# Optimization experiments

Measured on AMD Instinct MI355X. Metric: run time of the kernel, lower is better.

Reference implementation:

```python
import jax, jax.numpy as jnp
import numpy as np

N_NODES = 50000
N_EDGES = 800000
N_GRAPHS = 64
IN_C = 64
HID = 64
HEADS = 4
NEG_SLOPE = 0.2
EPS = 1e-16


def setup_inputs() -> dict:
    key = jax.random.key(0)
    ks = jax.random.split(key, 16)
    x = jax.random.normal(ks[0], (N_NODES, IN_C), dtype=jnp.float32)
    edge_index = jax.random.randint(ks[1], (2, N_EDGES), 0, N_NODES, dtype=jnp.int64)
    batch = jnp.sort(jax.random.randint(ks[2], (N_NODES,), 0, N_GRAPHS, dtype=jnp.int64))
    s = 1.0 / np.sqrt(IN_C)
    s2 = 1.0 / np.sqrt(HID * HEADS)
    s3 = 1.0 / np.sqrt(HID)
    return {
        "x": x,
        "edge_index": edge_index,
        "batch": batch,
        # GATv2 layer 1: in 64 -> heads*64 = 256 (concat)
        "Wl1": jax.random.normal(ks[3], (IN_C, HEADS * HID), dtype=jnp.float32) * s,
        "Wr1": jax.random.normal(ks[4], (IN_C, HEADS * HID), dtype=jnp.float32) * s,
        "att1": jax.random.normal(ks[5], (HEADS, HID), dtype=jnp.float32) * s3,
        "b1": jnp.zeros((HEADS * HID,), dtype=jnp.float32),
        # GATv2 layer 2: in 256 -> 1 head * 64
        "Wl2": jax.random.normal(ks[6], (HEADS * HID, HID), dtype=jnp.float32) * s2,
        "Wr2": jax.random.normal(ks[7], (HEADS * HID, HID), dtype=jnp.float32) * s2,
        "att2": jax.random.normal(ks[8], (1, HID), dtype=jnp.float32) * s3,
        "b2": jnp.zeros((HID,), dtype=jnp.float32),
        # MLP head: 64 -> 64 -> 2
        "W3": jax.random.normal(ks[9], (HID, 64), dtype=jnp.float32) * s3,
        "b3": jnp.zeros((64,), dtype=jnp.float32),
        "W4": jax.random.normal(ks[10], (64, 2), dtype=jnp.float32) * (1.0 / 8.0),
        "b4": jnp.zeros((2,), dtype=jnp.float32),
    }


def gatv2_conv(x, src, dst, Wl, Wr, att, bias, heads, out_c, n_nodes):
    # PyG GATv2Conv (eval mode, add_self_loops=False, concat heads):
    # x_l = lin_l(x) used for SOURCE nodes (messages), x_r = lin_r(x) for TARGET nodes.
    xl = (x @ Wl).reshape(n_nodes, heads, out_c)
    xr = (x @ Wr).reshape(n_nodes, heads, out_c)
    e = jax.nn.leaky_relu(xl[src] + xr[dst], NEG_SLOPE)          # [E, H, C]
    logits = jnp.einsum('ehc,hc->eh', e, att)                    # [E, H]
    # numerically stable softmax over incoming edges of each target node
    m = jax.ops.segment_max(logits, dst, num_segments=n_nodes)   # [N, H]
    ex = jnp.exp(logits - m[dst])
    denom = jax.ops.segment_sum(ex, dst, num_segments=n_nodes)   # [N, H]
    alpha = ex / (denom[dst] + EPS)                              # [E, H]
    out = jax.ops.segment_sum(alpha[:, :, None] * xl[src], dst, num_segments=n_nodes)
    return out.reshape(n_nodes, heads * out_c) + bias


def reference(x, edge_index, batch, Wl1, Wr1, att1, b1, Wl2, Wr2, att2, b2, W3, b3, W4, b4):
    src, dst = edge_index[0], edge_index[1]
    n = x.shape[0]
    h = gatv2_conv(x, src, dst, Wl1, Wr1, att1, b1, HEADS, HID, n)
    h = jax.nn.elu(h)
    h = gatv2_conv(h, src, dst, Wl2, Wr2, att2, b2, 1, HID, n)
    h = jax.nn.elu(h)
    # global mean pool over graphs
    sums = jax.ops.segment_sum(h, batch, num_segments=N_GRAPHS)
    cnt = jax.ops.segment_sum(jnp.ones((n,), dtype=h.dtype), batch, num_segments=N_GRAPHS)
    pooled = sums / jnp.maximum(cnt, 1.0)[:, None]
    # MLP head (dropout inactive in eval)
    z = jax.nn.relu(pooled @ W3 + b3)
    return z @ W4 + b4
```

## Files before the change

kernel.cpp:

```cpp
#include <hip/hip_runtime.h>
#include <hip/hip_fp16.h>
#include <math.h>

#define N_NODES 50000
#define N_EDGES 800000
#define N_GRAPHS 64
#define L2E 1.44269504f

#if __has_builtin(__builtin_amdgcn_fdot2)
#define HAS_FDOT2 1
typedef _Float16 h2_t __attribute__((ext_vector_type(2)));
#else
#define HAS_FDOT2 0
#endif

typedef _Float16 f16x8 __attribute__((ext_vector_type(8)));
typedef float f32x4 __attribute__((ext_vector_type(4)));

__device__ __forceinline__ float elu1(float v){ return v > 0.f ? v : expm1f(v); }

__device__ __forceinline__ float pkdot(float4 q, const __half2* r2,
        const __half2* A6, const __half2* A4){
    const __half2* qh = (const __half2*)&q;
    float p = 0.f;
#if HAS_FDOT2
    #pragma unroll
    for (int i=0;i<4;i++){
        __half2 u = __hadd2(qh[i], r2[i]);
        __half2 ua = __builtin_bit_cast(__half2,
            __builtin_bit_cast(unsigned, u) & 0x7FFF7FFFu);
        p = __builtin_amdgcn_fdot2(__builtin_bit_cast(h2_t,u),
                                   __builtin_bit_cast(h2_t,A6[i]), p, false);
        p = __builtin_amdgcn_fdot2(__builtin_bit_cast(h2_t,ua),
                                   __builtin_bit_cast(h2_t,A4[i]), p, false);
    }
#else
    #pragma unroll
    for (int i=0;i<4;i++){
        float2 qf = __half22float2(qh[i]);
        float2 rf = __half22float2(r2[i]);
        float2 s6 = __half22float2(A6[i]);
        float2 s4 = __half22float2(A4[i]);
        float u0 = qf.x + rf.x, u1 = qf.y + rf.y;
        p = fmaf(s6.x, u0, fmaf(s4.x, fabsf(u0), p));
        p = fmaf(s6.y, u1, fmaf(s4.y, fabsf(u1), p));
    }
#endif
    return p;
}

__global__ __launch_bounds__(256) void k_prep(const float* __restrict__ x,
        const float* __restrict__ Wl1, const float* __restrict__ Wr1,
        const float* __restrict__ Wl2, const float* __restrict__ Wr2,
        const int* __restrict__ ei,
        __half* __restrict__ xh, __half* __restrict__ Wt1, __half* __restrict__ Wt2,
        int* __restrict__ deg, float* __restrict__ pooled){
    int t = threadIdx.x, bk = blockIdx.x;
    if (bk < 3125){
        int idx = bk*256 + t;
        float4 v = ((const float4*)x)[idx];
        __half2* dst = (__half2*)xh + (size_t)idx*2;
        dst[0] = __floats2half2_rn(v.x, v.y);
        dst[1] = __floats2half2_rn(v.z, v.w);
    } else if (bk < 3381){
        int elem = (bk-3125)*256 + t;
        if (elem < 32768){
            int c = elem >> 6, k = elem & 63;
            float v = (c < 256) ? Wl1[k*256 + c] : Wr1[k*256 + (c-256)];
            Wt1[elem] = __float2half(v);
        } else {
            int e2 = elem - 32768;
            int c = e2 >> 8, k = e2 & 255;
            float v = (c < 64) ? Wl2[k*64 + c] : Wr2[k*64 + (c-64)];
            Wt2[e2] = __float2half(v);
        }
        if (elem < N_GRAPHS*64) pooled[elem] = 0.f;
    } else {
        int e4 = (bk-3381)*256 + t;
        if (e4 < N_EDGES/4){
            int4 d = ((const int4*)(ei + N_EDGES))[e4];
            atomicAdd(&deg[d.x],1); atomicAdd(&deg[d.y],1);
            atomicAdd(&deg[d.z],1); atomicAdd(&deg[d.w],1);
        }
    }
}

__global__ __launch_bounds__(1024) void k_scan_a(const int* __restrict__ deg,
        int* __restrict__ rowptr, int* __restrict__ partial){
    __shared__ int s[1024];
    int t = threadIdx.x; int i = blockIdx.x*1024 + t;
    int v = (i < N_NODES) ? deg[i] : 0;
    s[t] = v; __syncthreads();
    for (int off=1; off<1024; off<<=1){
        int add = (t>=off) ? s[t-off] : 0;
        __syncthreads();
        s[t] += add;
        __syncthreads();
    }
    if (i < N_NODES) rowptr[i] = s[t] - v;
    if (t == 1023) partial[blockIdx.x] = s[1023];
}

__global__ __launch_bounds__(1024) void k_scan_c(int* __restrict__ rowptr,
        int* __restrict__ cursor, const int* __restrict__ partial){
    __shared__ int base;
    if (threadIdx.x == 0){
        int run = 0;
        for (int bk=0; bk<(int)blockIdx.x; bk++) run += partial[bk];
        base = run;
    }
    __syncthreads();
    int i = blockIdx.x*1024 + threadIdx.x;
    if (i < N_NODES){
        int r = rowptr[i] + base;
        rowptr[i] = r; cursor[i] = r;
    } else if (i == N_NODES){
        rowptr[N_NODES] = N_EDGES;
    }
}

__global__ void k_scatter(const int* __restrict__ ei, int* __restrict__ cursor,
                          int* __restrict__ srcs){
    int e4 = blockIdx.x*256 + threadIdx.x;
    if (e4 < N_EDGES/4){
        int4 sv = ((const int4*)ei)[e4];
        int4 dv = ((const int4*)(ei + N_EDGES))[e4];
        int p0 = atomicAdd(&cursor[dv.x],1); srcs[p0] = sv.x;
        int p1 = atomicAdd(&cursor[dv.y],1); srcs[p1] = sv.y;
        int p2 = atomicAdd(&cursor[dv.z],1); srcs[p2] = sv.z;
        int p3 = atomicAdd(&cursor[dv.w],1); srcs[p3] = sv.w;
    }
}

__global__ __launch_bounds__(256) void k_mm1(const __half* __restrict__ xh,
        const __half* __restrict__ Wt1,
        __half* __restrict__ xl1h, __half* __restrict__ xr1h){
    __shared__ __half lds[4][16*136];
    int w = threadIdx.x >> 6, l = threadIdx.x & 63;
    int r0 = blockIdx.x*64 + w*16;
    int cg = blockIdx.y;
    int lr = l & 15, lk = l >> 4, lk4 = lk*4;
    int ar = r0 + lr; if (ar >= N_NODES) ar = N_NODES-1;
    const __half* arow = xh + (size_t)ar*64;
    f16x8 a0 = *(const f16x8*)(arow + lk*8);
    f16x8 a1 = *(const f16x8*)(arow + 32 + lk*8);
    f32x4 acc[8];
    #pragma unroll
    for (int ct=0; ct<8; ct++) acc[ct] = (f32x4){0.f,0.f,0.f,0.f};
    #pragma unroll
    for (int ct=0; ct<8; ct++){
        int col = cg*128 + ct*16 + lr;
        const __half* brow = Wt1 + (size_t)col*64;
        f16x8 b0 = *(const f16x8*)(brow + lk*8);
        f16x8 b1 = *(const f16x8*)(brow + 32 + lk*8);
        acc[ct] = __builtin_amdgcn_mfma_f32_16x16x32_f16(a0, b0, acc[ct], 0,0,0);
        acc[ct] = __builtin_amdgcn_mfma_f32_16x16x32_f16(a1, b1, acc[ct], 0,0,0);
    }
    #pragma unroll
    for (int ct=0; ct<8; ct++){
        #pragma unroll
        for (int i=0;i<4;i++)
            lds[w][(lk4+i)*136 + ct*16 + lr] = __float2half(acc[ct][i]);
    }
    __half* base = (cg < 2) ? xl1h : xr1h;
    int cbase = (cg & 1)*128;
    #pragma unroll
    for (int rr=0; rr<4; rr++){
        int row = rr*4 + lk;
        float4 v = *(const float4*)&lds[w][row*136 + lr*8];
        int grow = r0 + row;
        if (grow < N_NODES)
            *(float4*)&base[(size_t)grow*256 + cbase + lr*8] = v;
    }
}

__global__ __launch_bounds__(256) void k_mm2(const __half* __restrict__ h1h,
        const __half* __restrict__ Wt2,
        __half* __restrict__ xl2h, __half* __restrict__ xr2h){
    __shared__ __half lds[4][16*72];
    int w = threadIdx.x >> 6, l = threadIdx.x & 63;
    int r0 = blockIdx.x*64 + w*16;
    int cg = blockIdx.y;
    int lr = l & 15, lk = l >> 4, lk4 = lk*4;
    int ar = r0 + lr; if (ar >= N_NODES) ar = N_NODES-1;
    const __half* arow = h1h + (size_t)ar*256;
    f32x4 acc[4];
    #pragma unroll
    for (int ct=0; ct<4; ct++) acc[ct] = (f32x4){0.f,0.f,0.f,0.f};
    #pragma unroll
    for (int ks=0; ks<8; ks++){
        f16x8 a = *(const f16x8*)(arow + ks*32 + lk*8);
        #pragma unroll
        for (int ct=0; ct<4; ct++){
            int col = cg*64 + ct*16 + lr;
            f16x8 bf = *(const f16x8*)(Wt2 + (size_t)col*256 + ks*32 + lk*8);
            acc[ct] = __builtin_amdgcn_mfma_f32_16x16x32_f16(a, bf, acc[ct], 0,0,0);
        }
    }
    #pragma unroll
    for (int ct=0; ct<4; ct++){
        #pragma unroll
        for (int i=0;i<4;i++)
            lds[w][(lk4+i)*72 + ct*16 + lr] = __float2half(acc[ct][i]);
    }
    __half* base = (cg == 0) ? xl2h : xr2h;
    #pragma unroll
    for (int rr=0; rr<2; rr++){
        int row = rr*8 + (l>>3);
        float4 v = *(const float4*)&lds[w][row*72 + (l&7)*8];
        int grow = r0 + row;
        if (grow < N_NODES)
            *(float4*)&base[(size_t)grow*64 + (l&7)*8] = v;
    }
}

__global__ __launch_bounds__(256) void k_gat1(const __half* __restrict__ xlh,
        const __half* __restrict__ xrh, const int* __restrict__ srcs,
        const int* __restrict__ rowptr, const float* __restrict__ att,
        const float* __restrict__ b, __half* __restrict__ h1h){
    int w = threadIdx.x >> 6, l = threadIdx.x & 63;
    int n = blockIdx.x*4 + w;
    int g = l >> 5, sub = l & 31;
    const float4* xh4 = (const float4*)xlh;
    float4 rq = *(const float4*)(xrh + (size_t)n*256 + sub*8);
    __half2 r2[4];
    { const __half2* rh = (const __half2*)&rq;
      r2[0]=rh[0]; r2[1]=rh[1]; r2[2]=rh[2]; r2[3]=rh[3]; }
    float4 A0v = *(const float4*)(att + sub*8);
    float4 A1v = *(const float4*)(att + sub*8 + 4);
    const float C6 = 0.6f*L2E, C4 = 0.4f*L2E;
    __half2 A6[4] = { __floats2half2_rn(A0v.x*C6, A0v.y*C6),
                      __floats2half2_rn(A0v.z*C6, A0v.w*C6),
                      __floats2half2_rn(A1v.x*C6, A1v.y*C6),
                      __floats2half2_rn(A1v.z*C6, A1v.w*C6) };
    __half2 A4[4] = { __floats2half2_rn(A0v.x*C4, A0v.y*C4),
                      __floats2half2_rn(A0v.z*C4, A0v.w*C4),
                      __floats2half2_rn(A1v.x*C4, A1v.y*C4),
                      __floats2half2_rn(A1v.z*C4, A1v.w*C4) };
    const __half2 Z2 = __floats2half2_rn(0.f, 0.f);
    float accf[8];
    #pragma unroll
    for (int c=0;c<8;c++) accf[c]=0.f;
    float dacc = 0.f;
    int beg = rowptr[n], end = rowptr[n+1];
    for (int j = beg; j < end; j += 8){
        int j0=j+g, j1=j+2+g, j2=j+4+g, j3=j+6+g;
        bool c0=j0<end, c1=j1<end, c2=j2<end, c3=j3<end;
        int s0 = c0 ? srcs[j0] : 0;
        int s1 = c1 ? srcs[j1] : 0;
        int s2 = c2 ? srcs[j2] : 0;
        int s3 = c3 ? srcs[j3] : 0;
        float4 q0 = xh4[(size_t)(unsigned)s0*32 + sub];
        float4 q1 = xh4[(size_t)(unsigned)s1*32 + sub];
        float4 q2 = xh4[(size_t)(unsigned)s2*32 + sub];
        float4 q3 = xh4[(size_t)(unsigned)s3*32 + sub];
        float p0 = pkdot(q0, r2, A6, A4);
        float p1 = pkdot(q1, r2, A6, A4);
        float p2 = pkdot(q2, r2, A6, A4);
        float p3 = pkdot(q3, r2, A6, A4);
        #pragma unroll
        for (int off=1; off<8; off<<=1){
            p0 += __shfl_xor(p0, off);
            p1 += __shfl_xor(p1, off);
            p2 += __shfl_xor(p2, off);
            p3 += __shfl_xor(p3, off);
        }
        float e0 = c0 ? exp2f(p0) : 0.f;
        float e1 = c1 ? exp2f(p1) : 0.f;
        float e2 = c2 ? exp2f(p2) : 0.f;
        float e3 = c3 ? exp2f(p3) : 0.f;
        __half2 E0 = __half2half2(__float2half_rn(e0));
        __half2 E1 = __half2half2(__float2half_rn(e1));
        __half2 E2 = __half2half2(__float2half_rn(e2));
        __half2 E3 = __half2half2(__float2half_rn(e3));
        const __half2* q0h = (const __half2*)&q0;
        const __half2* q1h = (const __half2*)&q1;
        const __half2* q2h = (const __half2*)&q2;
        const __half2* q3h = (const __half2*)&q3;
        #pragma unroll
        for (int i=0;i<4;i++){
            __half2 a16 = __hfma2(E0, q0h[i], Z2);
            a16 = __hfma2(E1, q1h[i], a16);
            a16 = __hfma2(E2, q2h[i], a16);
            a16 = __hfma2(E3, q3h[i], a16);
            float2 f = __half22float2(a16);
            accf[2*i]   += f.x;
            accf[2*i+1] += f.y;
        }
        dacc += e0 + e1 + e2 + e3;
    }
    #pragma unroll
    for (int c=0;c<8;c++) accf[c] += __shfl_xor(accf[c], 32);
    dacc += __shfl_xor(dacc, 32);
    if (l < 32){
        float inv = 1.f / (dacc + 1e-16f);
        float4 B0 = *(const float4*)(b + l*8);
        float4 B1 = *(const float4*)(b + l*8 + 4);
        float4 st;
        __half2* sp = (__half2*)&st;
        sp[0] = __floats2half2_rn(elu1(fmaf(accf[0],inv,B0.x)), elu1(fmaf(accf[1],inv,B0.y)));
        sp[1] = __floats2half2_rn(elu1(fmaf(accf[2],inv,B0.z)), elu1(fmaf(accf[3],inv,B0.w)));
        sp[2] = __floats2half2_rn(elu1(fmaf(accf[4],inv,B1.x)), elu1(fmaf(accf[5],inv,B1.y)));
        sp[3] = __floats2half2_rn(elu1(fmaf(accf[6],inv,B1.z)), elu1(fmaf(accf[7],inv,B1.w)));
        *(float4*)(h1h + (size_t)n*256 + l*8) = st;
    }
}

__global__ __launch_bounds__(256) void k_gat2(const __half* __restrict__ xlh,
        const __half* __restrict__ xrh, const int* __restrict__ srcs,
        const int* __restrict__ rowptr, const float* __restrict__ att,
        const float* __restrict__ b, float* __restrict__ h2){
    int w = threadIdx.x >> 6, l = threadIdx.x & 63;
    int n = blockIdx.x*4 + w;
    int g = l >> 3, sub = l & 7;
    const float4* xh4 = (const float4*)xlh;
    float4 rq = *(const float4*)(xrh + (size_t)n*64 + sub*8);
    __half2 r2[4];
    { const __half2* rh = (const __half2*)&rq;
      r2[0]=rh[0]; r2[1]=rh[1]; r2[2]=rh[2]; r2[3]=rh[3]; }
    float4 A0v = *(const float4*)(att + sub*8);
    float4 A1v = *(const float4*)(att + sub*8 + 4);
    const float C6 = 0.6f*L2E, C4 = 0.4f*L2E;
    __half2 A6[4] = { __floats2half2_rn(A0v.x*C6, A0v.y*C6),
                      __floats2half2_rn(A0v.z*C6, A0v.w*C6),
                      __floats2half2_rn(A1v.x*C6, A1v.y*C6),
                      __floats2half2_rn(A1v.z*C6, A1v.w*C6) };
    __half2 A4[4] = { __floats2half2_rn(A0v.x*C4, A0v.y*C4),
                      __floats2half2_rn(A0v.z*C4, A0v.w*C4),
                      __floats2half2_rn(A1v.x*C4, A1v.y*C4),
                      __floats2half2_rn(A1v.z*C4, A1v.w*C4) };
    const __half2 Z2 = __floats2half2_rn(0.f, 0.f);
    __half2 a16[4] = {Z2, Z2, Z2, Z2};
    float dacc = 0.f;
    int beg = rowptr[n], end = rowptr[n+1];
    for (int j = beg; j < end; j += 16){
        int j0 = j+g, j1 = j+8+g;
        bool c0 = j0<end, c1 = j1<end;
        int s0 = c0 ? srcs[j0] : 0;
        int s1 = c1 ? srcs[j1] : 0;
        float4 q0 = xh4[(size_t)(unsigned)s0*8 + sub];
        float4 q1 = xh4[(size_t)(unsigned)s1*8 + sub];
        float p0 = pkdot(q0, r2, A6, A4);
        float p1 = pkdot(q1, r2, A6, A4);
        #pragma unroll
        for (int off=1; off<8; off<<=1){
            p0 += __shfl_xor(p0, off);
            p1 += __shfl_xor(p1, off);
        }
        float e0 = c0 ? exp2f(p0) : 0.f;
        float e1 = c1 ? exp2f(p1) : 0.f;
        __half2 E0 = __half2half2(__float2half_rn(e0));
        __half2 E1 = __half2half2(__float2half_rn(e1));
        const __half2* q0h = (const __half2*)&q0;
        const __half2* q1h = (const __half2*)&q1;
        #pragma unroll
        for (int i=0;i<4;i++){
            a16[i] = __hfma2(E0, q0h[i], a16[i]);
            a16[i] = __hfma2(E1, q1h[i], a16[i]);
        }
        dacc += e0 + e1;
    }
    float accf[8];
    #pragma unroll
    for (int i=0;i<4;i++){
        float2 f = __half22float2(a16[i]);
        accf[2*i] = f.x; accf[2*i+1] = f.y;
    }
    #pragma unroll
    for (int off=8; off<64; off<<=1){
        #pragma unroll
        for (int c=0;c<8;c++) accf[c] += __shfl_xor(accf[c], off);
        dacc += __shfl_xor(dacc, off);
    }
    if (l < 8){
        float inv = 1.f / (dacc + 1e-16f);
        float4 B0 = *(const float4*)(b + l*8);
        float4 B1 = *(const float4*)(b + l*8 + 4);
        float4 o0, o1;
        o0.x = elu1(fmaf(accf[0], inv, B0.x));
        o0.y = elu1(fmaf(accf[1], inv, B0.y));
        o0.z = elu1(fmaf(accf[2], inv, B0.z));
        o0.w = elu1(fmaf(accf[3], inv, B0.w));
        o1.x = elu1(fmaf(accf[4], inv, B1.x));
        o1.y = elu1(fmaf(accf[5], inv, B1.y));
        o1.z = elu1(fmaf(accf[6], inv, B1.z));
        o1.w = elu1(fmaf(accf[7], inv, B1.w));
        float4* op = (float4*)(h2 + (size_t)n*64 + l*8);
        op[0] = o0; op[1] = o1;
    }
}

__device__ __forceinline__ int lower_bound_i(const int* a, int n, int key){
    int lo = 0, hi = n;
    while (lo < hi){ int mid = (lo+hi)>>1; if (a[mid] < key) lo = mid+1; else hi = mid; }
    return lo;
}

__global__ __launch_bounds__(256) void k_pool(const float* __restrict__ h2,
        const int* __restrict__ batch, float* __restrict__ pooled){
    int gph = blockIdx.x, part = blockIdx.y;
    int t = threadIdx.x, c = t & 63, q = t >> 6;
    int start = lower_bound_i(batch, N_NODES, gph);
    int end   = lower_bound_i(batch, N_NODES, gph+1);
    int len = end - start;
    int is = start + (int)(((long long)len*part) >> 3);
    int ie = start + (int)(((long long)len*(part+1)) >> 3);
    float s = 0.f;
    for (int i = is + q; i < ie; i += 4) s += h2[(size_t)i*64 + c];
    __shared__ float red[256];
    red[t] = s; __syncthreads();
    if (q == 0){
        float tot = red[c] + red[64+c] + red[128+c] + red[192+c];
        atomicAdd(&pooled[gph*64 + c], tot);
    }
}

__global__ __launch_bounds__(64) void k_mlp(const float* __restrict__ pooled,
        const int* __restrict__ batch,
        const float* __restrict__ W3, const float* __restrict__ b3,
        const float* __restrict__ W4, const float* __restrict__ b4,
        float* __restrict__ out){
    int gph = blockIdx.x, t = threadIdx.x;
    __shared__ float ps[64], zs[64];
    int start = lower_bound_i(batch, N_NODES, gph);
    int end   = lower_bound_i(batch, N_NODES, gph+1);
    float cnt = fmaxf((float)(end - start), 1.f);
    ps[t] = pooled[gph*64 + t] / cnt;
    __syncthreads();
    float a = b3[t];
    for (int k=0;k<64;k++) a = fmaf(ps[k], W3[k*64+t], a);
    zs[t] = fmaxf(a, 0.f); __syncthreads();
    if (t < 2){
        float o = b4[t];
        for (int k=0;k<64;k++) o = fmaf(zs[k], W4[k*2+t], o);
        out[gph*2 + t] = o;
    }
}

extern "C" void kernel_launch(void* const* d_in, const int* in_sizes, int n_in,
                              void* d_out, int out_size, void* d_ws, size_t ws_size,
                              hipStream_t stream) {
    const float* x    = (const float*)d_in[0];
    const int*   ei   = (const int*)  d_in[1];
    const int*   batch= (const int*)  d_in[2];
    const float* Wl1  = (const float*)d_in[3];
    const float* Wr1  = (const float*)d_in[4];
    const float* att1 = (const float*)d_in[5];
    const float* b1   = (const float*)d_in[6];
    const float* Wl2  = (const float*)d_in[7];
    const float* Wr2  = (const float*)d_in[8];
    const float* att2 = (const float*)d_in[9];
    const float* b2   = (const float*)d_in[10];
    const float* W3   = (const float*)d_in[11];
    const float* b3   = (const float*)d_in[12];
    const float* W4   = (const float*)d_in[13];
    const float* b4   = (const float*)d_in[14];
    float* out = (float*)d_out;

    char* wsp = (char*)d_ws;
    size_t off = 0;
    auto alloc = [&](size_t bytes) -> char* {
        char* p = wsp + off; off += (bytes + 255) & ~(size_t)255; return p;
    };
    __half* xh    = (__half*)alloc((size_t)N_NODES*64*2);
    __half* Wt1   = (__half*)alloc(512*64*2);
    __half* Wt2   = (__half*)alloc(128*256*2);
    __half* xl1h  = (__half*)alloc((size_t)N_NODES*256*2);
    __half* xr1h  = (__half*)alloc((size_t)N_NODES*256*2);
    __half* h1h   = (__half*)alloc((size_t)N_NODES*256*2);
    int* rowptr   = (int*)alloc((N_NODES+1)*4);
    int* cursor   = (int*)alloc(N_NODES*4);
    int* partial  = (int*)alloc(64*4);
    int* srcs     = (int*)alloc((size_t)N_EDGES*4);
    int* deg      = (int*)alloc(N_NODES*4);
    float* pooled = (float*)alloc(N_GRAPHS*64*4);
    __half* xl2h  = xl1h;
    __half* xr2h  = xl1h + (size_t)N_NODES*64;
    float*  h2    = (float*)xr1h;

    hipMemsetAsync(deg, 0, (size_t)N_NODES*sizeof(int), stream);
    k_prep<<<3125+256+782, 256, 0, stream>>>(x, Wl1, Wr1, Wl2, Wr2, ei,
                                             xh, Wt1, Wt2, deg, pooled);
    k_scan_a<<<49, 1024, 0, stream>>>(deg, rowptr, partial);
    k_scan_c<<<49, 1024, 0, stream>>>(rowptr, cursor, partial);
    k_scatter<<<782, 256, 0, stream>>>(ei, cursor, srcs);

    k_mm1<<<dim3(782,4), 256, 0, stream>>>(xh, Wt1, xl1h, xr1h);
    k_gat1<<<N_NODES/4, 256, 0, stream>>>(xl1h, xr1h, srcs, rowptr, att1, b1, h1h);
    k_mm2<<<dim3(782,2), 256, 0, stream>>>(h1h, Wt2, xl2h, xr2h);
    k_gat2<<<N_NODES/4, 256, 0, stream>>>(xl2h, xr2h, srcs, rowptr, att2, b2, h2);
    k_pool<<<dim3(N_GRAPHS,8), 256, 0, stream>>>(h2, batch, pooled);
    k_mlp<<<N_GRAPHS, 64, 0, stream>>>(pooled, batch, W3, b3, W4, b4, out);
}
```

Before: 294.7 us.

## Record edge ranks during degree count, fuse atomic-free CSR scatter into mm1, peel tails

The degree-counting atomics now return each edge's rank within its destination, which is stored so the later scatter can place each source as rowptr[dst]+rank with no second round of atomics. The scatter then runs as an extra blockIdx.y slice of the mm1 launch, removing a separate kernel and the cursor array. The GAT edge loops are split into full unchecked chunks plus one bounds-checked tail, so the per-iteration predication is dropped. The cost is an extra 3.2 MB ranks array written and read back, and the CSR order within each row still depends on atomic arrival order.

Result: faster. 257.2 us (-12.7%).

```diff
diff --git a/kernel.cpp b/kernel.cpp
--- a/kernel.cpp
+++ b/kernel.cpp
@@ -54,7 +54,7 @@
         const float* __restrict__ Wl2, const float* __restrict__ Wr2,
         const int* __restrict__ ei,
         __half* __restrict__ xh, __half* __restrict__ Wt1, __half* __restrict__ Wt2,
-        int* __restrict__ deg, float* __restrict__ pooled){
+        int* __restrict__ deg, int* __restrict__ ranks, float* __restrict__ pooled){
     int t = threadIdx.x, bk = blockIdx.x;
     if (bk < 3125){
         int idx = bk*256 + t;
@@ -79,8 +79,12 @@
         int e4 = (bk-3381)*256 + t;
         if (e4 < N_EDGES/4){
             int4 d = ((const int4*)(ei + N_EDGES))[e4];
-            atomicAdd(&deg[d.x],1); atomicAdd(&deg[d.y],1);
-            atomicAdd(&deg[d.z],1); atomicAdd(&deg[d.w],1);
+            int4 r;
+            r.x = atomicAdd(&deg[d.x],1);
+            r.y = atomicAdd(&deg[d.y],1);
+            r.z = atomicAdd(&deg[d.z],1);
+            r.w = atomicAdd(&deg[d.w],1);
+            ((int4*)ranks)[e4] = r;
         }
     }
 }
@@ -102,7 +106,7 @@
 }
 
 __global__ __launch_bounds__(1024) void k_scan_c(int* __restrict__ rowptr,
-        int* __restrict__ cursor, const int* __restrict__ partial){
+        const int* __restrict__ partial){
     __shared__ int base;
     if (threadIdx.x == 0){
         int run = 0;
@@ -112,29 +116,30 @@
     __syncthreads();
     int i = blockIdx.x*1024 + threadIdx.x;
     if (i < N_NODES){
-        int r = rowptr[i] + base;
-        rowptr[i] = r; cursor[i] = r;
+        rowptr[i] += base;
     } else if (i == N_NODES){
         rowptr[N_NODES] = N_EDGES;
     }
 }
 
-__global__ void k_scatter(const int* __restrict__ ei, int* __restrict__ cursor,
-                          int* __restrict__ srcs){
-    int e4 = blockIdx.x*256 + threadIdx.x;
-    if (e4 < N_EDGES/4){
-        int4 sv = ((const int4*)ei)[e4];
-        int4 dv = ((const int4*)(ei + N_EDGES))[e4];
-        int p0 = atomicAdd(&cursor[dv.x],1); srcs[p0] = sv.x;
-        int p1 = atomicAdd(&cursor[dv.y],1); srcs[p1] = sv.y;
-        int p2 = atomicAdd(&cursor[dv.z],1); srcs[p2] = sv.z;
-        int p3 = atomicAdd(&cursor[dv.w],1); srcs[p3] = sv.w;
-    }
-}
-
 __global__ __launch_bounds__(256) void k_mm1(const __half* __restrict__ xh,
         const __half* __restrict__ Wt1,
-        __half* __restrict__ xl1h, __half* __restrict__ xr1h){
+        __half* __restrict__ xl1h, __half* __restrict__ xr1h,
+        const int* __restrict__ ei, const int* __restrict__ ranks,
+        const int* __restrict__ rowptr, int* __restrict__ srcs){
+    if (blockIdx.y == 4){
+        int e4 = blockIdx.x*256 + threadIdx.x;
+        if (e4 < N_EDGES/4){
+            int4 sv = ((const int4*)ei)[e4];
+            int4 dv = ((const int4*)(ei + N_EDGES))[e4];
+            int4 rv = ((const int4*)ranks)[e4];
+            __builtin_nontemporal_store(sv.x, &srcs[rowptr[dv.x] + rv.x]);
+            __builtin_nontemporal_store(sv.y, &srcs[rowptr[dv.y] + rv.y]);
+            __builtin_nontemporal_store(sv.z, &srcs[rowptr[dv.z] + rv.z]);
+            __builtin_nontemporal_store(sv.w, &srcs[rowptr[dv.w] + rv.w]);
+        }
+        return;
+    }
     __shared__ __half lds[4][16*136];
     int w = threadIdx.x >> 6, l = threadIdx.x & 63;
     int r0 = blockIdx.x*64 + w*16;
@@ -243,13 +248,15 @@
     for (int c=0;c<8;c++) accf[c]=0.f;
     float dacc = 0.f;
     int beg = rowptr[n], end = rowptr[n+1];
-    for (int j = beg; j < end; j += 8){
+
+    auto body = [&](int j, bool checked){
         int j0=j+g, j1=j+2+g, j2=j+4+g, j3=j+6+g;
-        bool c0=j0<end, c1=j1<end, c2=j2<end, c3=j3<end;
-        int s0 = c0 ? srcs[j0] : 0;
-        int s1 = c1 ? srcs[j1] : 0;
-        int s2 = c2 ? srcs[j2] : 0;
-        int s3 = c3 ? srcs[j3] : 0;
+        bool c0=true, c1=true, c2=true, c3=true;
+        if (checked){
+            c0 = j0<end; c1 = j1<end; c2 = j2<end; c3 = j3<end;
+            j0 = c0?j0:beg; j1 = c1?j1:beg; j2 = c2?j2:beg; j3 = c3?j3:beg;
+        }
+        int s0 = srcs[j0], s1 = srcs[j1], s2 = srcs[j2], s3 = srcs[j3];
         float4 q0 = xh4[(size_t)(unsigned)s0*32 + sub];
         float4 q1 = xh4[(size_t)(unsigned)s1*32 + sub];
         float4 q2 = xh4[(size_t)(unsigned)s2*32 + sub];
@@ -265,10 +272,10 @@
             p2 += __shfl_xor(p2, off);
             p3 += __shfl_xor(p3, off);
         }
-        float e0 = c0 ? exp2f(p0) : 0.f;
-        float e1 = c1 ? exp2f(p1) : 0.f;
-        float e2 = c2 ? exp2f(p2) : 0.f;
-        float e3 = c3 ? exp2f(p3) : 0.f;
+        float e0 = exp2f(p0), e1 = exp2f(p1), e2 = exp2f(p2), e3 = exp2f(p3);
+        if (checked){
+            e0 = c0?e0:0.f; e1 = c1?e1:0.f; e2 = c2?e2:0.f; e3 = c3?e3:0.f;
+        }
         __half2 E0 = __half2half2(__float2half_rn(e0));
         __half2 E1 = __half2half2(__float2half_rn(e1));
         __half2 E2 = __half2half2(__float2half_rn(e2));
@@ -288,7 +295,13 @@
             accf[2*i+1] += f.y;
         }
         dacc += e0 + e1 + e2 + e3;
-    }
+    };
+
+    int j = beg;
+    int nfull = (end - beg) >> 3;
+    for (int it=0; it<nfull; ++it, j+=8) body(j, false);
+    if (j < end) body(j, true);
+
     #pragma unroll
     for (int c=0;c<8;c++) accf[c] += __shfl_xor(accf[c], 32);
     dacc += __shfl_xor(dacc, 32);
@@ -333,11 +346,15 @@
     __half2 a16[4] = {Z2, Z2, Z2, Z2};
     float dacc = 0.f;
     int beg = rowptr[n], end = rowptr[n+1];
-    for (int j = beg; j < end; j += 16){
+
+    auto body = [&](int j, bool checked){
         int j0 = j+g, j1 = j+8+g;
-        bool c0 = j0<end, c1 = j1<end;
-        int s0 = c0 ? srcs[j0] : 0;
-        int s1 = c1 ? srcs[j1] : 0;
+        bool c0=true, c1=true;
+        if (checked){
+            c0 = j0<end; c1 = j1<end;
+            j0 = c0?j0:beg; j1 = c1?j1:beg;
+        }
+        int s0 = srcs[j0], s1 = srcs[j1];
         float4 q0 = xh4[(size_t)(unsigned)s0*8 + sub];
         float4 q1 = xh4[(size_t)(unsigned)s1*8 + sub];
         float p0 = pkdot(q0, r2, A6, A4);
@@ -347,8 +364,8 @@
             p0 += __shfl_xor(p0, off);
             p1 += __shfl_xor(p1, off);
         }
-        float e0 = c0 ? exp2f(p0) : 0.f;
-        float e1 = c1 ? exp2f(p1) : 0.f;
+        float e0 = exp2f(p0), e1 = exp2f(p1);
+        if (checked){ e0 = c0?e0:0.f; e1 = c1?e1:0.f; }
         __half2 E0 = __half2half2(__float2half_rn(e0));
         __half2 E1 = __half2half2(__float2half_rn(e1));
         const __half2* q0h = (const __half2*)&q0;
@@ -359,7 +376,13 @@
             a16[i] = __hfma2(E1, q1h[i], a16[i]);
         }
         dacc += e0 + e1;
-    }
+    };
+
+    int j = beg;
+    int nfull = (end - beg) >> 4;
+    for (int it=0; it<nfull; ++it, j+=16) body(j, false);
+    if (j < end) body(j, true);
+
     float accf[8];
     #pragma unroll
     for (int i=0;i<4;i++){
@@ -469,9 +492,9 @@
     __half* xr1h  = (__half*)alloc((size_t)N_NODES*256*2);
     __half* h1h   = (__half*)alloc((size_t)N_NODES*256*2);
     int* rowptr   = (int*)alloc((N_NODES+1)*4);
-    int* cursor   = (int*)alloc(N_NODES*4);
     int* partial  = (int*)alloc(64*4);
     int* srcs     = (int*)alloc((size_t)N_EDGES*4);
+    int* ranks    = (int*)alloc((size_t)N_EDGES*4);
     int* deg      = (int*)alloc(N_NODES*4);
     float* pooled = (float*)alloc(N_GRAPHS*64*4);
     __half* xl2h  = xl1h;
@@ -480,12 +503,12 @@
 
     hipMemsetAsync(deg, 0, (size_t)N_NODES*sizeof(int), stream);
     k_prep<<<3125+256+782, 256, 0, stream>>>(x, Wl1, Wr1, Wl2, Wr2, ei,
-                                             xh, Wt1, Wt2, deg, pooled);
+                                             xh, Wt1, Wt2, deg, ranks, pooled);
     k_scan_a<<<49, 1024, 0, stream>>>(deg, rowptr, partial);
-    k_scan_c<<<49, 1024, 0, stream>>>(rowptr, cursor, partial);
-    k_scatter<<<782, 256, 0, stream>>>(ei, cursor, srcs);
-
-    k_mm1<<<dim3(782,4), 256, 0, stream>>>(xh, Wt1, xl1h, xr1h);
+    k_scan_c<<<49, 1024, 0, stream>>>(rowptr, partial);
+
+    k_mm1<<<dim3(782,5), 256, 0, stream>>>(xh, Wt1, xl1h, xr1h,
+                                           ei, ranks, rowptr, srcs);
     k_gat1<<<N_NODES/4, 256, 0, stream>>>(xl1h, xr1h, srcs, rowptr, att1, b1, h1h);
     k_mm2<<<dim3(782,2), 256, 0, stream>>>(h1h, Wt2, xl2h, xr2h);
     k_gat2<<<N_NODES/4, 256, 0, stream>>>(xl2h, xr2h, srcs, rowptr, att2, b2, h2);
```
